# Kernel tuning notes

Measured on AMD Instinct MI355X. Metric: run time of the kernel, lower is better.

## Reference

```python
import jax, jax.numpy as jnp
import numpy as np

N_QUBITS = 14
D = 2 ** N_QUBITS            # 16384 state dim
E = 2048                     # embedding_dim
N_PAIRS = N_QUBITS * (N_QUBITS - 1) // 2  # 91


def _linear_init(key, fan_in, fan_out):
    kw, kb = jax.random.split(key)
    bound = 1.0 / np.sqrt(fan_in)
    w = jax.random.uniform(kw, (fan_in, fan_out), jnp.float32, -bound, bound)
    b = jax.random.uniform(kb, (fan_out,), jnp.float32, -bound, bound)
    return w, b


def setup_inputs() -> dict:
    key = jax.random.key(0)
    ks = jax.random.split(key, 12)
    qs_real = jax.random.normal(ks[0], (D,), jnp.float32) * 0.1
    qs_imag = jax.random.normal(ks[1], (D,), jnp.float32) * 0.1
    amp_w1, amp_b1 = _linear_init(ks[2], 2 * D, E)
    amp_w2, amp_b2 = _linear_init(ks[3], E, E)
    ln_g = jnp.ones((E,), jnp.float32)
    ln_b = jnp.zeros((E,), jnp.float32)
    ph_w1, ph_b1 = _linear_init(ks[4], D, E // 2)
    ph_w2, ph_b2 = _linear_init(ks[5], E // 2, E // 2)
    ent_w1, ent_b1 = _linear_init(ks[6], N_PAIRS, E // 4)
    ent_w2, ent_b2 = _linear_init(ks[7], E // 4, E // 4)
    fus_w, fus_b = _linear_init(ks[8], E + E // 2 + E // 4, E)
    return dict(qs_real=qs_real, qs_imag=qs_imag,
                amp_w1=amp_w1, amp_b1=amp_b1, amp_w2=amp_w2, amp_b2=amp_b2,
                ln_g=ln_g, ln_b=ln_b,
                ph_w1=ph_w1, ph_b1=ph_b1, ph_w2=ph_w2, ph_b2=ph_b2,
                ent_w1=ent_w1, ent_b1=ent_b1, ent_w2=ent_w2, ent_b2=ent_b2,
                fus_w=fus_w, fus_b=fus_b, n_qubits=N_QUBITS)


def _layer_norm(x, g, b, eps=1e-5):
    m = jnp.mean(x)
    v = jnp.mean(jnp.square(x - m))
    return (x - m) / jnp.sqrt(v + eps) * g + b


def _entanglement_features(re, im, n_qubits):
    # abs(sum(state[::2^(n-i-1)] * state[1::2^(n-j-1)])) for all pairs i<j,
    # slices truncated to common length 2^(i+1); complex arithmetic via re/im.
    feats = []
    for i in range(n_qubits):
        si = 2 ** (n_qubits - i - 1)
        L = 2 ** (i + 1)
        a, b = re[::si], im[::si]          # length 2^(i+1)
        for j in range(i + 1, n_qubits):
            sj = 2 ** (n_qubits - j - 1)
            c, d = re[1::sj][:L], im[1::sj][:L]
            rr = jnp.sum(a * c - b * d)
            ii = jnp.sum(a * d + b * c)
            feats.append(jnp.sqrt(rr * rr + ii * ii))
    return jnp.stack(feats)


def reference(qs_real, qs_imag,
              amp_w1, amp_b1, amp_w2, amp_b2, ln_g, ln_b,
              ph_w1, ph_b1, ph_w2, ph_b2,
              ent_w1, ent_b1, ent_w2, ent_b2,
              fus_w, fus_b, n_qubits):
    # normalize the complex state
    norm = jnp.sqrt(jnp.sum(qs_real * qs_real + qs_imag * qs_imag))
    re = qs_real / norm
    im = qs_imag / norm
    phases = jnp.arctan2(im, re)
    # amplitude encoder on [real; imag]
    x = jnp.concatenate([re, im])
    a = jax.nn.relu(x @ amp_w1 + amp_b1) @ amp_w2 + amp_b2
    amp_emb = _layer_norm(a, ln_g, ln_b)
    # phase encoder
    ph_emb = jax.nn.relu(phases @ ph_w1 + ph_b1) @ ph_w2 + ph_b2
    # entanglement encoder
    ef = _entanglement_features(re, im, int(n_qubits))
    ent_emb = jax.nn.relu(ef @ ent_w1 + ent_b1) @ ent_w2 + ent_b2
    combined = jnp.concatenate([amp_emb, ph_emb, ent_emb])
    return combined @ fus_w + fus_b
```

## Files before the change

kernel.cpp:

```cpp
#include <hip/hip_runtime.h>
#include <math.h>

#define DD 16384
#define NQ 14

__device__ __forceinline__ void atomAddF(float* p, float v) {
#if defined(__HIP_PLATFORM_AMD__)
    unsafeAtomicAdd(p, v);
#else
    atomicAdd(p, v);
#endif
}

__global__ __launch_bounds__(256) void k_norm(const float4* __restrict__ qr4,
                                              const float4* __restrict__ qi4,
                                              float* __restrict__ sum) {
    __shared__ float sred[4];
    int t = blockIdx.x * 256 + threadIdx.x;
    float4 r = qr4[t], m = qi4[t];
    float v = r.x * r.x + r.y * r.y + r.z * r.z + r.w * r.w +
              m.x * m.x + m.y * m.y + m.z * m.z + m.w * m.w;
#pragma unroll
    for (int off = 32; off; off >>= 1) v += __shfl_down(v, off);
    if ((threadIdx.x & 63) == 0) sred[threadIdx.x >> 6] = v;
    __syncthreads();
    if (threadIdx.x == 0) atomAddF(sum, sred[0] + sred[1] + sred[2] + sred[3]);
}

__global__ __launch_bounds__(256) void k_prep(const float4* __restrict__ qr4,
                                              const float4* __restrict__ qi4,
                                              const float* __restrict__ sum,
                                              float4* __restrict__ x4,
                                              float4* __restrict__ ph4) {
    int t = blockIdx.x * 256 + threadIdx.x;
    float inv = 1.0f / sqrtf(*sum);
    float4 r = qr4[t], m = qi4[t];
    float4 xr = {r.x * inv, r.y * inv, r.z * inv, r.w * inv};
    float4 xi = {m.x * inv, m.y * inv, m.z * inv, m.w * inv};
    x4[t] = xr;
    x4[DD / 4 + t] = xi;
    float4 p = {atan2f(m.x, r.x), atan2f(m.y, r.y), atan2f(m.z, r.z), atan2f(m.w, r.w)};
    ph4[t] = p;
}

__global__ __launch_bounds__(512, 4) void k_matvec(const float* __restrict__ W,
                                                   const float* __restrict__ xpre,
                                                   const float* __restrict__ xbias, int act,
                                                   float* __restrict__ acc,
                                                   const float* __restrict__ obias,
                                                   int C4, int R, int rpc) {
    __shared__ float sx[128];
    int chunk = blockIdx.x;
    int r0 = chunk * rpc;
    int nr = min(rpc, R - r0);
    for (int i = threadIdx.x; i < nr; i += blockDim.x) {
        float v = xpre[r0 + i];
        if (act) v = fmaxf(v + xbias[r0 + i], 0.0f);
        sx[i] = v;
    }
    __syncthreads();
    const float4* __restrict__ Wp =
        reinterpret_cast<const float4*>(W) + (size_t)r0 * C4 + threadIdx.x;
    float ax = 0.f, ay = 0.f, az = 0.f, aw = 0.f;
    float bx = 0.f, by = 0.f, bz = 0.f, bw = 0.f;
    int i = 0;
    for (; i + 8 <= nr; i += 8) {
        float4 w0 = Wp[0];
        float4 w1 = Wp[(size_t)C4 * 1];
        float4 w2 = Wp[(size_t)C4 * 2];
        float4 w3 = Wp[(size_t)C4 * 3];
        float4 w4 = Wp[(size_t)C4 * 4];
        float4 w5 = Wp[(size_t)C4 * 5];
        float4 w6 = Wp[(size_t)C4 * 6];
        float4 w7 = Wp[(size_t)C4 * 7];
        float x0 = sx[i + 0], x1 = sx[i + 1], x2 = sx[i + 2], x3 = sx[i + 3];
        float x4 = sx[i + 4], x5 = sx[i + 5], x6 = sx[i + 6], x7 = sx[i + 7];
        ax = fmaf(x0, w0.x, ax); ay = fmaf(x0, w0.y, ay); az = fmaf(x0, w0.z, az); aw = fmaf(x0, w0.w, aw);
        bx = fmaf(x1, w1.x, bx); by = fmaf(x1, w1.y, by); bz = fmaf(x1, w1.z, bz); bw = fmaf(x1, w1.w, bw);
        ax = fmaf(x2, w2.x, ax); ay = fmaf(x2, w2.y, ay); az = fmaf(x2, w2.z, az); aw = fmaf(x2, w2.w, aw);
        bx = fmaf(x3, w3.x, bx); by = fmaf(x3, w3.y, by); bz = fmaf(x3, w3.z, bz); bw = fmaf(x3, w3.w, bw);
        ax = fmaf(x4, w4.x, ax); ay = fmaf(x4, w4.y, ay); az = fmaf(x4, w4.z, az); aw = fmaf(x4, w4.w, aw);
        bx = fmaf(x5, w5.x, bx); by = fmaf(x5, w5.y, by); bz = fmaf(x5, w5.z, bz); bw = fmaf(x5, w5.w, bw);
        ax = fmaf(x6, w6.x, ax); ay = fmaf(x6, w6.y, ay); az = fmaf(x6, w6.z, az); aw = fmaf(x6, w6.w, aw);
        bx = fmaf(x7, w7.x, bx); by = fmaf(x7, w7.y, by); bz = fmaf(x7, w7.z, bz); bw = fmaf(x7, w7.w, bw);
        Wp += (size_t)C4 * 8;
    }
    for (; i < nr; i++) {
        float4 w = *Wp;
        Wp += C4;
        float xv = sx[i];
        ax = fmaf(xv, w.x, ax); ay = fmaf(xv, w.y, ay);
        az = fmaf(xv, w.z, az); aw = fmaf(xv, w.w, aw);
    }
    ax += bx; ay += by; az += bz; aw += bw;
    int col = threadIdx.x * 4;
    if (chunk == 0 && obias) {
        ax += obias[col + 0]; ay += obias[col + 1];
        az += obias[col + 2]; aw += obias[col + 3];
    }
    atomAddF(&acc[col + 0], ax);
    atomAddF(&acc[col + 1], ay);
    atomAddF(&acc[col + 2], az);
    atomAddF(&acc[col + 3], aw);
}

__global__ __launch_bounds__(512) void k_ln(const float* __restrict__ a,
                                            const float* __restrict__ b2,
                                            const float* __restrict__ g,
                                            const float* __restrict__ bb,
                                            float* __restrict__ out) {
    __shared__ float s1[8], s2[8];
    int tid = threadIdx.x;
    float v[4];
    float s = 0.f;
#pragma unroll
    for (int e = 0; e < 4; e++) {
        int idx = tid + 512 * e;
        v[e] = a[idx] + b2[idx];
        s += v[e];
    }
#pragma unroll
    for (int off = 32; off; off >>= 1) s += __shfl_down(s, off);
    if ((tid & 63) == 0) s1[tid >> 6] = s;
    __syncthreads();
    float tot = s1[0] + s1[1] + s1[2] + s1[3] + s1[4] + s1[5] + s1[6] + s1[7];
    float mean = tot * (1.0f / 2048.0f);
    float q = 0.f;
#pragma unroll
    for (int e = 0; e < 4; e++) {
        float d = v[e] - mean;
        q += d * d;
    }
#pragma unroll
    for (int off = 32; off; off >>= 1) q += __shfl_down(q, off);
    if ((tid & 63) == 0) s2[tid >> 6] = q;
    __syncthreads();
    float tv = s2[0] + s2[1] + s2[2] + s2[3] + s2[4] + s2[5] + s2[6] + s2[7];
    float var = tv * (1.0f / 2048.0f);
    float inv = 1.0f / sqrtf(var + 1e-5f);
#pragma unroll
    for (int e = 0; e < 4; e++) {
        int idx = tid + 512 * e;
        out[idx] = (v[e] - mean) * inv * g[idx] + bb[idx];
    }
}

__global__ __launch_bounds__(256) void k_efeat(const float* __restrict__ x,
                                               float* __restrict__ ef) {
    __shared__ float srr[4], sii[4];
    int p = blockIdx.x;
    int i = 0, rem = p;
    while (rem >= (NQ - 1) - i) { rem -= (NQ - 1) - i; i++; }
    int j = i + 1 + rem;
    int si = 1 << (NQ - i - 1);
    int sj = 1 << (NQ - j - 1);
    int L = 1 << (i + 1);
    const float* re = x;
    const float* im = x + DD;
    float rr = 0.f, ii = 0.f;
    for (int k = threadIdx.x; k < L; k += 256) {
        float a = re[k * si], b = im[k * si];
        float c = re[1 + k * sj], d = im[1 + k * sj];
        rr += a * c - b * d;
        ii += a * d + b * c;
    }
#pragma unroll
    for (int off = 32; off; off >>= 1) {
        rr += __shfl_down(rr, off);
        ii += __shfl_down(ii, off);
    }
    if ((threadIdx.x & 63) == 0) {
        srr[threadIdx.x >> 6] = rr;
        sii[threadIdx.x >> 6] = ii;
    }
    __syncthreads();
    if (threadIdx.x == 0) {
        float R = srr[0] + srr[1] + srr[2] + srr[3];
        float I = sii[0] + sii[1] + sii[2] + sii[3];
        ef[p] = sqrtf(R * R + I * I);
    }
}

extern "C" void kernel_launch(void* const* d_in, const int* in_sizes, int n_in,
                              void* d_out, int out_size, void* d_ws, size_t ws_size,
                              hipStream_t stream) {
    const float* qs_real = (const float*)d_in[0];
    const float* qs_imag = (const float*)d_in[1];
    const float* amp_w1  = (const float*)d_in[2];
    const float* amp_b1  = (const float*)d_in[3];
    const float* amp_w2  = (const float*)d_in[4];
    const float* amp_b2  = (const float*)d_in[5];
    const float* ln_g    = (const float*)d_in[6];
    const float* ln_b    = (const float*)d_in[7];
    const float* ph_w1   = (const float*)d_in[8];
    const float* ph_b1   = (const float*)d_in[9];
    const float* ph_w2   = (const float*)d_in[10];
    const float* ph_b2   = (const float*)d_in[11];
    const float* ent_w1  = (const float*)d_in[12];
    const float* ent_b1  = (const float*)d_in[13];
    const float* ent_w2  = (const float*)d_in[14];
    const float* ent_b2  = (const float*)d_in[15];
    const float* fus_w   = (const float*)d_in[16];
    const float* fus_b   = (const float*)d_in[17];
    float* out = (float*)d_out;
    float* ws = (float*)d_ws;

    const int o_sum  = 0;
    const int o_h1   = 1024;
    const int o_a    = 4096;
    const int o_p1   = 8192;
    const int o_ef   = 12288;
    const int o_eh1  = 13312;
    const int o_comb = 16384;
    const int o_x    = 20480;
    const int o_ph   = 53248;

    hipMemsetAsync(d_ws, 0, (size_t)(o_comb + 3584) * sizeof(float), stream);
    hipMemsetAsync(d_out, 0, 2048 * sizeof(float), stream);

    k_norm<<<16, 256, 0, stream>>>((const float4*)qs_real, (const float4*)qs_imag, ws + o_sum);
    k_prep<<<16, 256, 0, stream>>>((const float4*)qs_real, (const float4*)qs_imag,
                                   ws + o_sum, (float4*)(ws + o_x), (float4*)(ws + o_ph));

    k_matvec<<<256, 512, 0, stream>>>(amp_w1, ws + o_x, nullptr, 0, ws + o_h1, nullptr,
                                      512, 2 * DD, 128);
    k_matvec<<<256, 512, 0, stream>>>(amp_w2, ws + o_h1, amp_b1, 1, ws + o_a, nullptr,
                                      512, 2048, 8);
    k_ln<<<1, 512, 0, stream>>>(ws + o_a, amp_b2, ln_g, ln_b, ws + o_comb);

    k_matvec<<<512, 256, 0, stream>>>(ph_w1, ws + o_ph, nullptr, 0, ws + o_p1, nullptr,
                                      256, DD, 32);
    k_matvec<<<256, 256, 0, stream>>>(ph_w2, ws + o_p1, ph_b1, 1, ws + o_comb + 2048, ph_b2,
                                      256, 1024, 4);

    k_efeat<<<91, 256, 0, stream>>>(ws + o_x, ws + o_ef);
    k_matvec<<<4, 128, 0, stream>>>(ent_w1, ws + o_ef, nullptr, 0, ws + o_eh1, nullptr,
                                    128, 91, 23);
    k_matvec<<<16, 128, 0, stream>>>(ent_w2, ws + o_eh1, ent_b1, 1, ws + o_comb + 3072, ent_b2,
                                     128, 512, 32);

    k_matvec<<<256, 512, 0, stream>>>(fus_w, ws + o_comb, nullptr, 0, out, fus_b,
                                      512, 3584, 14);
}
```

Measured before the change: 637.6 us.

## Fuse normalization and atan2 prep into matvec loaders, split amp_w1 finer

```diff
diff --git a/kernel.cpp b/kernel.cpp
--- a/kernel.cpp
+++ b/kernel.cpp
@@ -3,6 +3,11 @@
 
 #define DD 16384
 #define NQ 14
+
+#define ACT_PLAIN   0
+#define ACT_RELU    1
+#define ACT_NORMCAT 2
+#define ACT_ATAN2   3
 
 __device__ __forceinline__ void atomAddF(float* p, float v) {
 #if defined(__HIP_PLATFORM_AMD__)
@@ -27,25 +32,11 @@
     if (threadIdx.x == 0) atomAddF(sum, sred[0] + sred[1] + sred[2] + sred[3]);
 }
 
-__global__ __launch_bounds__(256) void k_prep(const float4* __restrict__ qr4,
-                                              const float4* __restrict__ qi4,
-                                              const float* __restrict__ sum,
-                                              float4* __restrict__ x4,
-                                              float4* __restrict__ ph4) {
-    int t = blockIdx.x * 256 + threadIdx.x;
-    float inv = 1.0f / sqrtf(*sum);
-    float4 r = qr4[t], m = qi4[t];
-    float4 xr = {r.x * inv, r.y * inv, r.z * inv, r.w * inv};
-    float4 xi = {m.x * inv, m.y * inv, m.z * inv, m.w * inv};
-    x4[t] = xr;
-    x4[DD / 4 + t] = xi;
-    float4 p = {atan2f(m.x, r.x), atan2f(m.y, r.y), atan2f(m.z, r.z), atan2f(m.w, r.w)};
-    ph4[t] = p;
-}
-
 __global__ __launch_bounds__(512, 4) void k_matvec(const float* __restrict__ W,
-                                                   const float* __restrict__ xpre,
-                                                   const float* __restrict__ xbias, int act,
+                                                   const float* __restrict__ src0,
+                                                   const float* __restrict__ src1,
+                                                   const float* __restrict__ scalep,
+                                                   int act,
                                                    float* __restrict__ acc,
                                                    const float* __restrict__ obias,
                                                    int C4, int R, int rpc) {
@@ -53,9 +44,14 @@
     int chunk = blockIdx.x;
     int r0 = chunk * rpc;
     int nr = min(rpc, R - r0);
+    float scl = (act == ACT_NORMCAT) ? rsqrtf(*scalep) : 1.0f;
     for (int i = threadIdx.x; i < nr; i += blockDim.x) {
-        float v = xpre[r0 + i];
-        if (act) v = fmaxf(v + xbias[r0 + i], 0.0f);
+        int g = r0 + i;
+        float v;
+        if (act == ACT_RELU)         v = fmaxf(src0[g] + src1[g], 0.0f);
+        else if (act == ACT_NORMCAT) v = (g < DD ? src0[g] : src1[g - DD]) * scl;
+        else if (act == ACT_ATAN2)   v = atan2f(src1[g], src0[g]);
+        else                         v = src0[g];
         sx[i] = v;
     }
     __syncthreads();
@@ -145,7 +141,9 @@
     }
 }
 
-__global__ __launch_bounds__(256) void k_efeat(const float* __restrict__ x,
+__global__ __launch_bounds__(256) void k_efeat(const float* __restrict__ re,
+                                               const float* __restrict__ im,
+                                               const float* __restrict__ sump,
                                                float* __restrict__ ef) {
     __shared__ float srr[4], sii[4];
     int p = blockIdx.x;
@@ -155,8 +153,6 @@
     int si = 1 << (NQ - i - 1);
     int sj = 1 << (NQ - j - 1);
     int L = 1 << (i + 1);
-    const float* re = x;
-    const float* im = x + DD;
     float rr = 0.f, ii = 0.f;
     for (int k = threadIdx.x; k < L; k += 256) {
         float a = re[k * si], b = im[k * si];
@@ -177,7 +173,7 @@
     if (threadIdx.x == 0) {
         float R = srr[0] + srr[1] + srr[2] + srr[3];
         float I = sii[0] + sii[1] + sii[2] + sii[3];
-        ef[p] = sqrtf(R * R + I * I);
+        ef[p] = sqrtf(R * R + I * I) / (*sump);
     }
 }
 
@@ -212,33 +208,29 @@
     const int o_ef   = 12288;
     const int o_eh1  = 13312;
     const int o_comb = 16384;
-    const int o_x    = 20480;
-    const int o_ph   = 53248;
 
     hipMemsetAsync(d_ws, 0, (size_t)(o_comb + 3584) * sizeof(float), stream);
     hipMemsetAsync(d_out, 0, 2048 * sizeof(float), stream);
 
     k_norm<<<16, 256, 0, stream>>>((const float4*)qs_real, (const float4*)qs_imag, ws + o_sum);
-    k_prep<<<16, 256, 0, stream>>>((const float4*)qs_real, (const float4*)qs_imag,
-                                   ws + o_sum, (float4*)(ws + o_x), (float4*)(ws + o_ph));
-
-    k_matvec<<<256, 512, 0, stream>>>(amp_w1, ws + o_x, nullptr, 0, ws + o_h1, nullptr,
-                                      512, 2 * DD, 128);
-    k_matvec<<<256, 512, 0, stream>>>(amp_w2, ws + o_h1, amp_b1, 1, ws + o_a, nullptr,
-                                      512, 2048, 8);
+
+    k_matvec<<<512, 512, 0, stream>>>(amp_w1, qs_real, qs_imag, ws + o_sum, ACT_NORMCAT,
+                                      ws + o_h1, nullptr, 512, 2 * DD, 64);
+    k_matvec<<<256, 512, 0, stream>>>(amp_w2, ws + o_h1, amp_b1, nullptr, ACT_RELU,
+                                      ws + o_a, nullptr, 512, 2048, 8);
     k_ln<<<1, 512, 0, stream>>>(ws + o_a, amp_b2, ln_g, ln_b, ws + o_comb);
 
-    k_matvec<<<512, 256, 0, stream>>>(ph_w1, ws + o_ph, nullptr, 0, ws + o_p1, nullptr,
-                                      256, DD, 32);
-    k_matvec<<<256, 256, 0, stream>>>(ph_w2, ws + o_p1, ph_b1, 1, ws + o_comb + 2048, ph_b2,
-                                      256, 1024, 4);
-
-    k_efeat<<<91, 256, 0, stream>>>(ws + o_x, ws + o_ef);
-    k_matvec<<<4, 128, 0, stream>>>(ent_w1, ws + o_ef, nullptr, 0, ws + o_eh1, nullptr,
-                                    128, 91, 23);
-    k_matvec<<<16, 128, 0, stream>>>(ent_w2, ws + o_eh1, ent_b1, 1, ws + o_comb + 3072, ent_b2,
-                                     128, 512, 32);
-
-    k_matvec<<<256, 512, 0, stream>>>(fus_w, ws + o_comb, nullptr, 0, out, fus_b,
-                                      512, 3584, 14);
-}
+    k_matvec<<<512, 256, 0, stream>>>(ph_w1, qs_real, qs_imag, nullptr, ACT_ATAN2,
+                                      ws + o_p1, nullptr, 256, DD, 32);
+    k_matvec<<<256, 256, 0, stream>>>(ph_w2, ws + o_p1, ph_b1, nullptr, ACT_RELU,
+                                      ws + o_comb + 2048, ph_b2, 256, 1024, 4);
+
+    k_efeat<<<91, 256, 0, stream>>>(qs_real, qs_imag, ws + o_sum, ws + o_ef);
+    k_matvec<<<4, 128, 0, stream>>>(ent_w1, ws + o_ef, nullptr, nullptr, ACT_PLAIN,
+                                    ws + o_eh1, nullptr, 128, 91, 23);
+    k_matvec<<<16, 128, 0, stream>>>(ent_w2, ws + o_eh1, ent_b1, nullptr, ACT_RELU,
+                                     ws + o_comb + 3072, ent_b2, 128, 512, 32);
+
+    k_matvec<<<256, 512, 0, stream>>>(fus_w, ws + o_comb, nullptr, nullptr, ACT_PLAIN,
+                                      out, fus_b, 512, 3584, 14);
+}
```

Result: no change. 645.4 us (+1.2%).
